# Kernel tuning notes

Hardware: AMD Instinct MI355X
Metric: run time of the kernel (lower is better)

## Reference

```python
import jax, jax.numpy as jnp
import numpy as np

B, C, H, W = 8, 256, 32, 32
N = H * W  # 1024; conv1 maps C -> N channels so all bmms are [B,N,N]


def setup_inputs() -> dict:
    key = jax.random.key(0)
    ks = jax.random.split(key, 11)
    s = 0.02  # weight scale to keep softmax logits in a sane range
    return {
        "x":     jax.random.normal(ks[0], (B, C, H, W), jnp.float32),
        "w1":    jax.random.normal(ks[1], (N, C), jnp.float32) * s,
        "b1":    jax.random.normal(ks[2], (N,), jnp.float32) * s,
        "wq":    jax.random.normal(ks[3], (N, N), jnp.float32) * s,
        "bq":    jax.random.normal(ks[4], (N,), jnp.float32) * s,
        "wv":    jax.random.normal(ks[5], (N, N), jnp.float32) * s,
        "bv":    jax.random.normal(ks[6], (N,), jnp.float32) * s,
        "w2":    jax.random.normal(ks[7], (C, N), jnp.float32) * s,
        "b2":    jax.random.normal(ks[8], (C,), jnp.float32) * s,
        "alpha": jax.random.normal(ks[9], (1,), jnp.float32),
        "beta":  jax.random.normal(ks[10], (1,), jnp.float32),
    }


def reference(x, w1, b1, wq, bq, wv, bv, w2, b2, alpha, beta):
    b, c, h, w = x.shape
    n = h * w
    # 1x1 convs as channel matmuls
    x1 = jnp.einsum('bchw,nc->bnhw', x, w1) + b1[None, :, None, None]  # [B,N,H,W]
    g = (jnp.einsum('bnhw,mn->bmhw', x1, wq) + bq[None, :, None, None]).reshape(b, n, n)
    r = (jnp.einsum('bnhw,mn->bmhw', x1, wv) + bv[None, :, None, None]).reshape(b, n, n)
    xf = x1.reshape(b, n, n)          # m^T in the torch code: [B, N_chan, HW]
    m = xf.transpose(0, 2, 1)         # m: [B, HW, N_chan]
    # spatial attention: z_s = softmax(m^T @ g)
    z_s = jax.nn.softmax(jnp.matmul(xf, g), axis=-1)            # [B,N,N]
    # channel attention: z_c = softmax(g^T @ m)
    z_c = jax.nn.softmax(jnp.matmul(g.transpose(0, 2, 1), m), axis=-1)  # [B,N,N]
    p_s = jnp.matmul(z_s, r)                                    # [B,N,HW]
    p_c = jnp.matmul(z_c, m).transpose(0, 2, 1)                 # [B,N,HW]
    p = (alpha[0] * p_s + beta[0] * p_c).reshape(b, n, h, w)
    out = jnp.einsum('bnhw,cn->bchw', p, w2) + b2[None, :, None, None]
    return out
```

## Files before the change

### kernel.cpp

```cpp
#include <hip/hip_runtime.h>
#include <hip/hip_bf16.h>


typedef __attribute__((ext_vector_type(4))) float f4;
typedef __attribute__((ext_vector_type(8))) short s8;
typedef __attribute__((ext_vector_type(4))) unsigned short us4;
typedef __attribute__((ext_vector_type(8))) unsigned short us8;

__device__ __forceinline__ unsigned short f2bf(float f) {
    __hip_bfloat16 h = __float2bfloat16(f);
    return __builtin_bit_cast(unsigned short, h);
}

#define GAS(p) ((const __attribute__((address_space(1))) unsigned int*)(p))
#define LAS(p) ((__attribute__((address_space(3))) unsigned int*)(p))

__global__ __launch_bounds__(256) void conv_weights(
    const float* __restrict__ w1, const float* __restrict__ wq,
    const float* __restrict__ wv, const float* __restrict__ w2,
    unsigned short* __restrict__ w1b, unsigned short* __restrict__ wqb,
    unsigned short* __restrict__ wvb, unsigned short* __restrict__ w2b,
    const float* __restrict__ bq, const float* __restrict__ bv,
    float* __restrict__ biasqv)
{
    long i = (long)blockIdx.x * 256 + threadIdx.x;
    if (i >= 655360) {
        long j = i - 655360;
        if (j < 512) {
            f4 v = (j < 256) ? ((const f4*)bq)[j] : ((const f4*)bv)[j - 256];
            ((f4*)biasqv)[j] = v;
        }
        return;
    }
    const float* src; unsigned short* dst; long base;
    if (i < 65536)               { src = w1; dst = w1b; base = 0; }
    else if (i < 65536+262144)   { src = wq; dst = wqb; base = 65536; }
    else if (i < 65536+524288)   { src = wv; dst = wvb; base = 65536+262144; }
    else                         { src = w2; dst = w2b; base = 65536+524288; }
    long j = i - base;
    f4 v = ((const f4*)src)[j];
    us4 o;
    #pragma unroll
    for (int k = 0; k < 4; ++k) o[k] = f2bf(v[k]);
    ((us4*)dst)[j] = o;
}

__global__ __launch_bounds__(256) void transpose_x(
    const float* __restrict__ x, unsigned short* __restrict__ xT)
{
    __shared__ float tl[32][33];
    const int b  = blockIdx.z;
    const int q0 = blockIdx.x * 32;
    const int c0 = blockIdx.y * 32;
    const int tx = threadIdx.x & 31, ty = threadIdx.x >> 5;
    #pragma unroll
    for (int j = 0; j < 4; ++j)
        tl[ty + j*8][tx] = x[((long)(b*256 + c0 + ty + j*8))*1024 + q0 + tx];
    __syncthreads();
    #pragma unroll
    for (int j = 0; j < 4; ++j)
        xT[((long)(b*1024 + q0 + ty + j*8))*256 + c0 + tx] = f2bf(tl[tx][ty + j*8]);
}

template<int BIAS, int SPLIT>
__global__ __launch_bounds__(512, 2) void gemm8p(
    const unsigned short* __restrict__ A0, const unsigned short* __restrict__ Bt0,
    int lda, int ldb,
    void* __restrict__ Cv0, void* __restrict__ Cv1, int ldc,
    const float* __restrict__ bias)
{
    constexpr int NT = 16;
    __shared__ __align__(16) unsigned short As[2][2][8192];
    __shared__ __align__(16) unsigned short Bs[2][2][8192];

    const int gx = gridDim.x, gy = gridDim.y;
    const int nwg = gx * gy;
    int d = blockIdx.x + gx * blockIdx.y;
    int swz = (d & 7) * (nwg >> 3) + (d >> 3);
    const int bx = swz % gx;
    const int by = swz / gx;

    const int m0 = by * 256;
    const int n0 = bx * 256;
    const int t  = threadIdx.x;
    const int w  = t >> 6, l = t & 63;
    const int wr = w >> 2, wc = w & 3;
    const int lr = l & 15, lg = l >> 4;

    const unsigned short* Asrc = A0  + (long)m0 * lda;
    const unsigned short* Bsrc = Bt0 + (long)n0 * ldb;

    const int rl4 = l >> 2;
    const int gsw = ((l & 3) ^ ((l >> 3) & 3)) * 8;
    const int rsw = (lr >> 1) & 3;

    auto stage = [&](const unsigned short* src, int ld_, unsigned short* slot,
                     int sp, int kh) {
        #pragma unroll
        for (int i = 0; i < 2; ++i) {
            const int rb = i*128 + w*16;
            __builtin_amdgcn_global_load_lds(
                GAS(src + (long)(rb + rl4)*ld_ + sp*64 + kh*32 + gsw),
                LAS(slot + rb*32), 16, 0, 0);
        }
    };

    f4 acc[8][4];
    #pragma unroll
    for (int i = 0; i < 8; ++i)
        #pragma unroll
        for (int j = 0; j < 4; ++j) acc[i][j] = (f4){0.f, 0.f, 0.f, 0.f};

    s8 aF[4], bF[4];
    auto rdA = [&](int db, int kh, int mh) {
        #pragma unroll
        for (int m = 0; m < 4; ++m) {
            const int R = wr*128 + mh*64 + m*16 + lr;
            aF[m] = *(const s8*)&As[db][kh][R*32 + ((lg ^ rsw) * 8)];
        }
    };
    auto rdB = [&](int db, int kh) {
        #pragma unroll
        for (int n = 0; n < 4; ++n) {
            const int R = wc*64 + n*16 + lr;
            bF[n] = *(const s8*)&Bs[db][kh][R*32 + ((lg ^ rsw) * 8)];
        }
    };

#define MM8(MH)                                                                  \
    __builtin_amdgcn_s_setprio(1);                                               \
    _Pragma("unroll")                                                            \
    for (int m_ = 0; m_ < 4; ++m_)                                               \
        _Pragma("unroll")                                                        \
        for (int n_ = 0; n_ < 4; ++n_)                                           \
            acc[(MH)*4 + m_][n_] = __builtin_amdgcn_mfma_f32_16x16x32_bf16(      \
                aF[m_], bF[n_], acc[(MH)*4 + m_][n_], 0, 0, 0);                  \
    __builtin_amdgcn_s_setprio(0);

#define PH8(DB, KH, MH, RB, STG, VM)                                             \
    rdA(DB, KH, MH);                                                             \
    if (RB) rdB(DB, KH);                                                         \
    STG;                                                                         \
    __builtin_amdgcn_sched_barrier(0);                                           \
    __builtin_amdgcn_s_barrier();                                                \
    asm volatile("s_waitcnt lgkmcnt(0)" ::: "memory");                           \
    __builtin_amdgcn_sched_barrier(0);                                           \
    MM8(MH);                                                                     \
    VM;                                                                          \
    __builtin_amdgcn_s_barrier();

    stage(Asrc, lda, &As[0][0][0], 0, 0);
    stage(Bsrc, ldb, &Bs[0][0][0], 0, 0);
    stage(Asrc, lda, &As[0][1][0], 0, 1);
    stage(Bsrc, ldb, &Bs[0][1][0], 0, 1);
    stage(Asrc, lda, &As[1][0][0], 1, 0);
    stage(Bsrc, ldb, &Bs[1][0][0], 1, 0);
    asm volatile("s_waitcnt vmcnt(4)" ::: "memory");
    __builtin_amdgcn_sched_barrier(0);
    __builtin_amdgcn_s_barrier();

    for (int j = 0; j < NT/2; ++j) {
        const int tb = 2*j + 1;
        const int t2 = (2*j + 2) & (NT - 1);
        const int t3 = (2*j + 3) & (NT - 1);
        PH8(0,0,0, 1, stage(Asrc, lda, &As[1][1][0], tb, 1), (void)0)
        PH8(0,0,1, 0, stage(Bsrc, ldb, &Bs[1][1][0], tb, 1), (void)0)
        PH8(0,1,0, 1, stage(Asrc, lda, &As[0][0][0], t2, 0), (void)0)
        PH8(0,1,1, 0, stage(Bsrc, ldb, &Bs[0][0][0], t2, 0),
            asm volatile("s_waitcnt vmcnt(4)" ::: "memory"))
        PH8(1,0,0, 1, stage(Asrc, lda, &As[0][1][0], t2, 1), (void)0)
        PH8(1,0,1, 0, stage(Bsrc, ldb, &Bs[0][1][0], t2, 1), (void)0)
        PH8(1,1,0, 1, stage(Asrc, lda, &As[1][0][0], t3, 0), (void)0)
        PH8(1,1,1, 0, stage(Bsrc, ldb, &Bs[1][0][0], t3, 0),
            asm volatile("s_waitcnt vmcnt(4)" ::: "memory"))
    }
#undef PH8
#undef MM8

    void* Cd = Cv0; int nbase = n0;
    if (SPLIT && n0 >= 1024) { Cd = Cv1; nbase = n0 - 1024; }

    const int rbase = lg * 4;
    #pragma unroll
    for (int mi = 0; mi < 8; ++mi) {
        #pragma unroll
        for (int n = 0; n < 4; ++n) {
            const int row  = m0 + wr*128 + mi*16 + rbase;
            const int col  = nbase + wc*64 + n*16 + lr;
            const int bcol = n0    + wc*64 + n*16 + lr;
            #pragma unroll
            for (int j = 0; j < 4; ++j) {
                float v = acc[mi][n][j];
                if (BIAS == 2) v += bias[bcol];
                ((unsigned short*)Cd)[(long)(row + j)*ldc + col] = f2bf(v);
            }
        }
    }
}

template<int BIAS, int OUTF32, int SPLIT, int NPASS, int COLSUM>
__global__ __launch_bounds__(512, 2) void gemm256(
    const unsigned short* __restrict__ A0, const unsigned short* __restrict__ Bt0,
    const unsigned short* __restrict__ A1, const unsigned short* __restrict__ Bt1,
    long sA, long sB, int lda, int ldb,
    void* __restrict__ Cv0, void* __restrict__ Cv1, long sC, int ldc,
    const float* __restrict__ bias, int nt1, float* __restrict__ csp)
{
    __shared__ __align__(16) unsigned short As[3][16384];
    __shared__ __align__(16) unsigned short Bs[3][8192];

    const int gx = gridDim.x, gy = gridDim.y;
    const int nwg = gx * gy * gridDim.z;
    int d = blockIdx.x + gx * (blockIdx.y + gy * blockIdx.z);
    int swz = (d & 7) * (nwg >> 3) + (d >> 3);
    const int bx = swz % gx; int tq = swz / gx;
    const int by = tq % gy;  const int bz = tq / gy;

    const int b  = bz;
    const int m0 = by * 256;
    const int n0 = bx * 128;
    const int t  = threadIdx.x;
    const int w  = t >> 6, l = t & 63;
    const int wr = w >> 1, wc = w & 1;
    const int lr = l & 15, lg = l >> 4;

    const unsigned short* A0b = A0  + (long)b * sA;
    const unsigned short* B0b = Bt0 + (long)b * sB;
    const unsigned short* A1b = (NPASS > 1) ? A1  + (long)b * sA : nullptr;
    const unsigned short* B1b = (NPASS > 1) ? Bt1 + (long)b * sB : nullptr;

    const int rl  = l >> 3;
    const int gsw = ((l & 7) ^ (rl & 7)) * 8;

    const int NT = NPASS * nt1;

    auto stageA = [&](int sp, int bf) {
        const unsigned short* Ap = A0b; int kt = sp * 64;
        if (NPASS > 1 && sp >= nt1) { Ap = A1b; kt = (sp - nt1) * 64; }
        #pragma unroll
        for (int i = 0; i < 4; ++i) {
            const int rb = w*32 + i*8;
            __builtin_amdgcn_global_load_lds(GAS(Ap + (long)(m0 + rb + rl)*lda + kt + gsw),
                                             LAS(&As[bf][rb*64]), 16, 0, 0);
        }
    };
    auto stageB = [&](int sp, int bf) {
        const unsigned short* Bp = B0b; int kt = sp * 64;
        if (NPASS > 1 && sp >= nt1) { Bp = B1b; kt = (sp - nt1) * 64; }
        #pragma unroll
        for (int i = 0; i < 2; ++i) {
            const int rb = w*16 + i*8;
            __builtin_amdgcn_global_load_lds(GAS(Bp + (long)(n0 + rb + rl)*ldb + kt + gsw),
                                             LAS(&Bs[bf][rb*64]), 16, 0, 0);
        }
    };

    f4 acc[4][4];
    #pragma unroll
    for (int i = 0; i < 4; ++i)
        #pragma unroll
        for (int j = 0; j < 4; ++j) acc[i][j] = (f4){0.f, 0.f, 0.f, 0.f};

    stageA(0, 0); stageB(0, 0);
    stageA(1, 1); stageB(1, 1);
    asm volatile("s_waitcnt vmcnt(6)" ::: "memory");
    __builtin_amdgcn_sched_barrier(0);
    __builtin_amdgcn_s_barrier();

    s8 a0[4], b0[4], a1f[4], b1f[4];

    #pragma unroll
    for (int m = 0; m < 4; ++m) {
        const int R = wr*64 + m*16 + lr;
        a0[m] = *(const s8*)&As[0][R*64 + ((lg ^ (R & 7)) * 8)];
    }
    #pragma unroll
    for (int n = 0; n < 4; ++n) {
        const int R = wc*64 + n*16 + lr;
        b0[n] = *(const s8*)&Bs[0][R*64 + ((lg ^ (R & 7)) * 8)];
    }
    asm volatile("s_waitcnt lgkmcnt(0)" ::: "memory");
    __builtin_amdgcn_sched_barrier(0);

    int buf = 0;
    for (int s = 0; s < NT; ++s) {
        int bn = buf + 2; if (bn >= 3) bn -= 3;
        int bx1 = buf + 1; if (bx1 >= 3) bx1 -= 3;

        #pragma unroll
        for (int m = 0; m < 4; ++m) {
            const int R = wr*64 + m*16 + lr;
            a1f[m] = *(const s8*)&As[buf][R*64 + (((4 + lg) ^ (R & 7)) * 8)];
        }
        #pragma unroll
        for (int n = 0; n < 4; ++n) {
            const int R = wc*64 + n*16 + lr;
            b1f[n] = *(const s8*)&Bs[buf][R*64 + (((4 + lg) ^ (R & 7)) * 8)];
        }
        if (s + 2 < NT) stageA(s + 2, bn);
        __builtin_amdgcn_s_setprio(1);
        #pragma unroll
        for (int m = 0; m < 4; ++m)
            #pragma unroll
            for (int n = 0; n < 4; ++n)
                acc[m][n] = __builtin_amdgcn_mfma_f32_16x16x32_bf16(a0[m], b0[n], acc[m][n], 0, 0, 0);
        __builtin_amdgcn_s_setprio(0);
        asm volatile("s_waitcnt lgkmcnt(0)" ::: "memory");
        __builtin_amdgcn_sched_barrier(0);

        if (s + 1 < NT) {
            if (s + 2 < NT) asm volatile("s_waitcnt vmcnt(4)" ::: "memory");
            else            asm volatile("s_waitcnt vmcnt(0)" ::: "memory");
            __builtin_amdgcn_sched_barrier(0);
            __builtin_amdgcn_s_barrier();
            #pragma unroll
            for (int m = 0; m < 4; ++m) {
                const int R = wr*64 + m*16 + lr;
                a0[m] = *(const s8*)&As[bx1][R*64 + ((lg ^ (R & 7)) * 8)];
            }
            #pragma unroll
            for (int n = 0; n < 4; ++n) {
                const int R = wc*64 + n*16 + lr;
                b0[n] = *(const s8*)&Bs[bx1][R*64 + ((lg ^ (R & 7)) * 8)];
            }
            if (s + 2 < NT) stageB(s + 2, bn);
            __builtin_amdgcn_s_setprio(1);
            #pragma unroll
            for (int m = 0; m < 4; ++m)
                #pragma unroll
                for (int n = 0; n < 4; ++n)
                    acc[m][n] = __builtin_amdgcn_mfma_f32_16x16x32_bf16(a1f[m], b1f[n], acc[m][n], 0, 0, 0);
            __builtin_amdgcn_s_setprio(0);
            asm volatile("s_waitcnt lgkmcnt(0)" ::: "memory");
            __builtin_amdgcn_sched_barrier(0);
        } else {
            __builtin_amdgcn_s_setprio(1);
            #pragma unroll
            for (int m = 0; m < 4; ++m)
                #pragma unroll
                for (int n = 0; n < 4; ++n)
                    acc[m][n] = __builtin_amdgcn_mfma_f32_16x16x32_bf16(a1f[m], b1f[n], acc[m][n], 0, 0, 0);
            __builtin_amdgcn_s_setprio(0);
        }

        buf = bx1;
    }

    void* Cd = Cv0; int nbase = n0;
    if (SPLIT && n0 >= 1024) { Cd = Cv1; nbase = n0 - 1024; }

    const int rbase = lg * 4;
    #pragma unroll
    for (int m = 0; m < 4; ++m) {
        #pragma unroll
        for (int n = 0; n < 4; ++n) {
            const int row  = m0 + wr*64 + m*16 + rbase;
            const int col  = nbase + wc*64 + n*16 + lr;
            const int bcol = n0    + wc*64 + n*16 + lr;
            #pragma unroll
            for (int j = 0; j < 4; ++j) {
                float v = acc[m][n][j];
                if (BIAS == 1) v += bias[row + j];
                else if (BIAS == 2) v += bias[bcol];
                const long idx = (long)b*sC + (long)(row + j)*ldc + col;
                if (OUTF32) ((float*)Cd)[idx] = v;
                else ((unsigned short*)Cd)[idx] = f2bf(v);
            }
        }
    }

    if (COLSUM) {
        const int p = by*16 + wr*4 + lg;
        #pragma unroll
        for (int n = 0; n < 4; ++n) {
            float s = 0.f;
            #pragma unroll
            for (int m = 0; m < 4; ++m)
                #pragma unroll
                for (int j = 0; j < 4; ++j) s += __expf(acc[m][n][j]);
            const int col = n0 + wc*64 + n*16 + lr;
            csp[(long)p*8192 + b*1024 + col] = s;
        }
    }
}

template<int BIAS, int OUTF32, int NT1, int NBUF>
__global__ __launch_bounds__(256) void gemm_pipe(
    const unsigned short* __restrict__ A0, const unsigned short* __restrict__ Bt0,
    long sA, long sB, int lda, int ldb,
    void* __restrict__ Cv0, long sC, int ldc,
    const float* __restrict__ bias)
{
    constexpr int NT = NT1;
    __shared__ __align__(16) unsigned short As[NBUF][4096];
    __shared__ __align__(16) unsigned short Bs[NBUF][4096];

    const int gx = gridDim.x, gy = gridDim.y;
    const int nwg = gx * gy * gridDim.z;
    int d = blockIdx.x + gx * (blockIdx.y + gy * blockIdx.z);
    int swz = (d & 7) * (nwg >> 3) + (d >> 3);
    const int bx = swz % gx; int tq = swz / gx;
    const int by = tq % gy;  const int bz = tq / gy;

    const int b  = bz;
    const int m0 = by * 128;
    const int n0 = bx * 128;
    const int t  = threadIdx.x;
    const int w  = t >> 6, l = t & 63;
    const int wr = w >> 1, wc = w & 1;
    const int lr = l & 15;

    const unsigned short* A0b = A0  + (long)b * sA;
    const unsigned short* B0b = Bt0 + (long)b * sB;

    const int rA   = w*32 + (l >> 2);
    const int cswz = ((l & 3) ^ ((l >> 3) & 3)) * 8;
    const int swzr = (((l >> 4) ^ ((lr >> 1) & 3)) * 8);

    f4 acc[4][4];
    #pragma unroll
    for (int i = 0; i < 4; ++i)
        #pragma unroll
        for (int j = 0; j < 4; ++j) acc[i][j] = (f4){0.f, 0.f, 0.f, 0.f};

    auto stage = [&](int sp, int bf) {
        const int kt = sp * 32;
        __builtin_amdgcn_global_load_lds(GAS(A0b + (long)(m0 + rA     )*lda + kt + cswz), LAS(&As[bf][w*1024      ]), 16, 0, 0);
        __builtin_amdgcn_global_load_lds(GAS(A0b + (long)(m0 + rA + 16)*lda + kt + cswz), LAS(&As[bf][w*1024 + 512]), 16, 0, 0);
        __builtin_amdgcn_global_load_lds(GAS(B0b + (long)(n0 + rA     )*ldb + kt + cswz), LAS(&Bs[bf][w*1024      ]), 16, 0, 0);
        __builtin_amdgcn_global_load_lds(GAS(B0b + (long)(n0 + rA + 16)*ldb + kt + cswz), LAS(&Bs[bf][w*1024 + 512]), 16, 0, 0);
    };

    #pragma unroll
    for (int dpl = 0; dpl < NBUF - 1; ++dpl) stage(dpl, dpl);

    int buf = 0;
    for (int s = 0; s < NT; ++s) {
        if (NBUF >= 4 && s + 2 < NT) asm volatile("s_waitcnt vmcnt(8)" ::: "memory");
        else if (s + 1 < NT)         asm volatile("s_waitcnt vmcnt(4)" ::: "memory");
        else                         asm volatile("s_waitcnt vmcnt(0)" ::: "memory");
        __builtin_amdgcn_s_barrier();
        __builtin_amdgcn_sched_barrier(0);

        s8 aF[4], bF[4];
        #pragma unroll
        for (int m = 0; m < 4; ++m) aF[m] = *(const s8*)&As[buf][(wr*64 + m*16 + lr)*32 + swzr];
        #pragma unroll
        for (int n = 0; n < 4; ++n) bF[n] = *(const s8*)&Bs[buf][(wc*64 + n*16 + lr)*32 + swzr];

        if (s + NBUF - 1 < NT) {
            int bn = buf + NBUF - 1; if (bn >= NBUF) bn -= NBUF;
            stage(s + NBUF - 1, bn);
        }

        __builtin_amdgcn_s_setprio(1);
        #pragma unroll
        for (int m = 0; m < 4; ++m)
            #pragma unroll
            for (int n = 0; n < 4; ++n)
                acc[m][n] = __builtin_amdgcn_mfma_f32_16x16x32_bf16(aF[m], bF[n], acc[m][n], 0, 0, 0);
        __builtin_amdgcn_s_setprio(0);

        if (++buf == NBUF) buf = 0;
    }

    const int rbase = (l >> 4) * 4;
    #pragma unroll
    for (int m = 0; m < 4; ++m) {
        #pragma unroll
        for (int n = 0; n < 4; ++n) {
            const int row = m0 + wr*64 + m*16 + rbase;
            const int col = n0 + wc*64 + n*16 + lr;
            #pragma unroll
            for (int j = 0; j < 4; ++j) {
                float v = acc[m][n][j];
                if (BIAS == 1) v += bias[row + j];
                else if (BIAS == 2) v += bias[col];
                const long idx = (long)b*sC + (long)(row + j)*ldc + col;
                if (OUTF32) ((float*)Cv0)[idx] = v;
                else ((unsigned short*)Cv0)[idx] = f2bf(v);
            }
        }
    }
}

__global__ __launch_bounds__(256) void row_softmax(
    const float* __restrict__ S, unsigned short* __restrict__ Z,
    const float* __restrict__ scale_p)
{
    const int wid = threadIdx.x >> 6, l = threadIdx.x & 63;
    const long row = (long)blockIdx.x * 4 + wid;
    const float* src = S + row * 1024;
    f4 v[4];
    #pragma unroll
    for (int i = 0; i < 4; ++i) v[i] = *(const f4*)&src[(i*64 + l)*4];
    float m = -3.4e38f;
    #pragma unroll
    for (int i = 0; i < 4; ++i)
        #pragma unroll
        for (int j = 0; j < 4; ++j) m = fmaxf(m, v[i][j]);
    #pragma unroll
    for (int off = 32; off; off >>= 1) m = fmaxf(m, __shfl_xor(m, off));
    float s = 0.f;
    #pragma unroll
    for (int i = 0; i < 4; ++i)
        #pragma unroll
        for (int j = 0; j < 4; ++j) { v[i][j] = __expf(v[i][j] - m); s += v[i][j]; }
    #pragma unroll
    for (int off = 32; off; off >>= 1) s += __shfl_xor(s, off);
    const float c = scale_p[0] / s;
    #pragma unroll
    for (int i = 0; i < 4; ++i) {
        us4 o;
        #pragma unroll
        for (int j = 0; j < 4; ++j) o[j] = f2bf(v[i][j] * c);
        *(us4*)&Z[row*1024 + (long)(i*64 + l)*4] = o;
    }
}

__global__ __launch_bounds__(256) void col_reduce(
    const float* __restrict__ csp, float* __restrict__ cs)
{
    const int q = blockIdx.x * 256 + threadIdx.x;
    float s = 0.f;
    #pragma unroll
    for (int p = 0; p < 64; ++p) s += csp[(long)p*8192 + q];
    cs[q] = s;
}

__global__ __launch_bounds__(256) void col_write(
    const float* __restrict__ S, const float* __restrict__ cs,
    unsigned short* __restrict__ Z, const float* __restrict__ scale_p)
{
    __shared__ float tile[64][65];
    const int b  = blockIdx.z;
    const int q0 = blockIdx.x * 64;
    const int k0 = blockIdx.y * 64;
    const int t  = threadIdx.x;
    const float* Sb = S + (long)b * 1048576;
    const int tq = t & 15, tr = t >> 4;
    #pragma unroll
    for (int ii = 0; ii < 4; ++ii) {
        const int kr = tr + ii*16;
        f4 v = *(const f4*)&Sb[(long)(k0 + kr)*1024 + q0 + tq*4];
        tile[kr][tq*4+0] = v[0]; tile[kr][tq*4+1] = v[1];
        tile[kr][tq*4+2] = v[2]; tile[kr][tq*4+3] = v[3];
    }
    __syncthreads();
    const int qr = t >> 2, kp = t & 3;
    const int q = q0 + qr;
    const float inv = scale_p[0] / cs[b*1024 + q];
    unsigned short* Zb = Z + (long)b*1048576 + (long)q*1024 + k0 + kp*16;
    us8 o0, o1;
    #pragma unroll
    for (int e = 0; e < 8; ++e) o0[e] = f2bf(inv * __expf(tile[kp*16 + e][qr]));
    #pragma unroll
    for (int e = 0; e < 8; ++e) o1[e] = f2bf(inv * __expf(tile[kp*16 + 8 + e][qr]));
    *(us8*)&Zb[0] = o0;
    *(us8*)&Zb[8] = o1;
}

extern "C" void kernel_launch(void* const* d_in, const int* in_sizes, int n_in,
                              void* d_out, int out_size, void* d_ws, size_t ws_size,
                              hipStream_t stream)
{
    const float* x     = (const float*)d_in[0];
    const float* w1    = (const float*)d_in[1];
    const float* b1    = (const float*)d_in[2];
    const float* wq    = (const float*)d_in[3];
    const float* bq    = (const float*)d_in[4];
    const float* wv    = (const float*)d_in[5];
    const float* bv    = (const float*)d_in[6];
    const float* w2    = (const float*)d_in[7];
    const float* b2    = (const float*)d_in[8];
    const float* alpha = (const float*)d_in[9];
    const float* beta  = (const float*)d_in[10];
    float* out = (float*)d_out;

    char* ws = (char*)d_ws;
    size_t off = 0;
    auto alloc = [&](size_t bytes) -> void* {
        void* p = ws + off; off += (bytes + 255) & ~(size_t)255; return p;
    };
    unsigned short* w1b   = (unsigned short*)alloc(1024L*256*2);
    unsigned short* wqvb  = (unsigned short*)alloc(2048L*1024*2);
    unsigned short* w2b   = (unsigned short*)alloc(256L*1024*2);
    float*          biasqv= (float*)alloc(2048L*4);
    float*          cspv  = (float*)alloc(64L*8192*4);
    float*          csv   = (float*)alloc(8L*1024*4);
    unsigned short* xTb   = (unsigned short*)alloc(8L*1024*256*2);
    unsigned short* x1b   = (unsigned short*)alloc(8L*1024*1024*2);
    unsigned short* x1tb  = (unsigned short*)alloc(8L*1024*1024*2);
    unsigned short* gtb   = (unsigned short*)alloc(8L*1024*1024*2);
    unsigned short* rtb   = (unsigned short*)alloc(8L*1024*1024*2);
    float*          Sf    = (float*)alloc(8L*1024*1024*4);
    unsigned short* zsb = x1tb;
    unsigned short* zcb = gtb;
    unsigned short* Ptb = (unsigned short*)Sf;

    const long S1M = 1048576;

    conv_weights<<<2562, 256, 0, stream>>>(w1, wq, wv, w2, w1b, wqvb, wqvb + S1M, w2b, bq, bv, biasqv);
    transpose_x<<<dim3(32, 8, 8), 256, 0, stream>>>(x, xTb);

    gemm256<1,0,0,1,0><<<dim3(8, 4, 8), 512, 0, stream>>>(
        w1b, xTb, nullptr, nullptr, 0, 262144, 256, 256, x1b, nullptr, S1M, 1024, b1, 4, nullptr);
    gemm256<2,0,0,1,0><<<dim3(8, 32, 1), 512, 0, stream>>>(
        xTb, w1b, nullptr, nullptr, 0, 0, 256, 256, x1tb, nullptr, 0, 1024, b1, 4, nullptr);
    gemm8p<2,1><<<dim3(8, 32), 512, 0, stream>>>(
        x1tb, wqvb, 1024, 1024, gtb, rtb, 1024, biasqv);
    gemm256<0,1,0,1,1><<<dim3(8, 4, 8), 512, 0, stream>>>(
        x1b, gtb, nullptr, nullptr, S1M, S1M, 1024, 1024, Sf, nullptr, S1M, 1024, nullptr, 16, cspv);
    row_softmax<<<2048, 256, 0, stream>>>(Sf, zsb, alpha);
    col_reduce<<<32, 256, 0, stream>>>(cspv, csv);
    col_write<<<dim3(16, 16, 8), 256, 0, stream>>>(Sf, csv, zcb, beta);
    gemm256<0,0,0,2,0><<<dim3(8, 4, 8), 512, 0, stream>>>(
        rtb, zsb, zcb, x1b, S1M, S1M, 1024, 1024, Ptb, nullptr, S1M, 1024, nullptr, 16, nullptr);
    gemm_pipe<1,1,32,4><<<dim3(8, 2, 8), 256, 0, stream>>>(
        w2b, Ptb, 0, S1M, 1024, 1024, out, 262144, 1024, b2);
}
```

Before: 175.0 us.

## Fuse exp and softmax stats into score GEMM, defer normalization to dual GEMM

The score GEMM now applies exp in its epilogue, stores bf16 exponentials instead of fp32 scores, and emits partial row and column sums. A small stats_reduce kernel finishes those sums, and a transpose kernel produces the column-softmax operand. A new dual-accumulator GEMM applies the 1/rowsum and 1/colsum scaling, with alpha and beta, in its epilogue. Weight conversion and the x transpose are merged into one launch. This drops the fp32 score round-trip and the separate softmax passes. The risk is that exp without max-subtraction could overflow on larger logits, and the second GEMM now holds two accumulator sets, which raises register pressure.

```diff
diff --git a/kernel.cpp b/kernel.cpp
--- a/kernel.cpp
+++ b/kernel.cpp
@@ -11,55 +11,59 @@
     __hip_bfloat16 h = __float2bfloat16(f);
     return __builtin_bit_cast(unsigned short, h);
 }
+__device__ __forceinline__ float bf2f(unsigned short u) {
+    unsigned int x = ((unsigned int)u) << 16;
+    return __builtin_bit_cast(float, x);
+}
 
 #define GAS(p) ((const __attribute__((address_space(1))) unsigned int*)(p))
 #define LAS(p) ((__attribute__((address_space(3))) unsigned int*)(p))
 
-__global__ __launch_bounds__(256) void conv_weights(
+__global__ __launch_bounds__(256) void prep(
     const float* __restrict__ w1, const float* __restrict__ wq,
     const float* __restrict__ wv, const float* __restrict__ w2,
     unsigned short* __restrict__ w1b, unsigned short* __restrict__ wqb,
     unsigned short* __restrict__ wvb, unsigned short* __restrict__ w2b,
     const float* __restrict__ bq, const float* __restrict__ bv,
-    float* __restrict__ biasqv)
-{
-    long i = (long)blockIdx.x * 256 + threadIdx.x;
-    if (i >= 655360) {
-        long j = i - 655360;
-        if (j < 512) {
-            f4 v = (j < 256) ? ((const f4*)bq)[j] : ((const f4*)bv)[j - 256];
-            ((f4*)biasqv)[j] = v;
-        }
-        return;
-    }
-    const float* src; unsigned short* dst; long base;
-    if (i < 65536)               { src = w1; dst = w1b; base = 0; }
-    else if (i < 65536+262144)   { src = wq; dst = wqb; base = 65536; }
-    else if (i < 65536+524288)   { src = wv; dst = wvb; base = 65536+262144; }
-    else                         { src = w2; dst = w2b; base = 65536+524288; }
-    long j = i - base;
-    f4 v = ((const f4*)src)[j];
-    us4 o;
-    #pragma unroll
-    for (int k = 0; k < 4; ++k) o[k] = f2bf(v[k]);
-    ((us4*)dst)[j] = o;
-}
-
-__global__ __launch_bounds__(256) void transpose_x(
+    float* __restrict__ biasqv,
     const float* __restrict__ x, unsigned short* __restrict__ xT)
 {
     __shared__ float tl[32][33];
-    const int b  = blockIdx.z;
-    const int q0 = blockIdx.x * 32;
-    const int c0 = blockIdx.y * 32;
-    const int tx = threadIdx.x & 31, ty = threadIdx.x >> 5;
-    #pragma unroll
-    for (int j = 0; j < 4; ++j)
-        tl[ty + j*8][tx] = x[((long)(b*256 + c0 + ty + j*8))*1024 + q0 + tx];
-    __syncthreads();
-    #pragma unroll
-    for (int j = 0; j < 4; ++j)
-        xT[((long)(b*1024 + q0 + ty + j*8))*256 + c0 + tx] = f2bf(tl[tx][ty + j*8]);
+    if (blockIdx.x < 2562) {
+        long i = (long)blockIdx.x * 256 + threadIdx.x;
+        if (i >= 655360) {
+            long j = i - 655360;
+            if (j < 512) {
+                f4 v = (j < 256) ? ((const f4*)bq)[j] : ((const f4*)bv)[j - 256];
+                ((f4*)biasqv)[j] = v;
+            }
+            return;
+        }
+        const float* src; unsigned short* dst; long base;
+        if (i < 65536)               { src = w1; dst = w1b; base = 0; }
+        else if (i < 65536+262144)   { src = wq; dst = wqb; base = 65536; }
+        else if (i < 65536+524288)   { src = wv; dst = wvb; base = 65536+262144; }
+        else                         { src = w2; dst = w2b; base = 65536+524288; }
+        long j = i - base;
+        f4 v = ((const f4*)src)[j];
+        us4 o;
+        #pragma unroll
+        for (int k = 0; k < 4; ++k) o[k] = f2bf(v[k]);
+        ((us4*)dst)[j] = o;
+    } else {
+        const int idx = blockIdx.x - 2562;
+        const int q0 = (idx & 31) * 32;
+        const int c0 = ((idx >> 5) & 7) * 32;
+        const int b  = idx >> 8;
+        const int tx = threadIdx.x & 31, ty = threadIdx.x >> 5;
+        #pragma unroll
+        for (int j = 0; j < 4; ++j)
+            tl[ty + j*8][tx] = x[((long)(b*256 + c0 + ty + j*8))*1024 + q0 + tx];
+        __syncthreads();
+        #pragma unroll
+        for (int j = 0; j < 4; ++j)
+            xT[((long)(b*1024 + q0 + ty + j*8))*256 + c0 + tx] = f2bf(tl[tx][ty + j*8]);
+    }
 }
 
 template<int BIAS, int SPLIT>
@@ -198,13 +202,13 @@
     }
 }
 
-template<int BIAS, int OUTF32, int SPLIT, int NPASS, int COLSUM>
+template<int BIAS, int OUTF32, int STATS>
 __global__ __launch_bounds__(512, 2) void gemm256(
     const unsigned short* __restrict__ A0, const unsigned short* __restrict__ Bt0,
-    const unsigned short* __restrict__ A1, const unsigned short* __restrict__ Bt1,
     long sA, long sB, int lda, int ldb,
-    void* __restrict__ Cv0, void* __restrict__ Cv1, long sC, int ldc,
-    const float* __restrict__ bias, int nt1, float* __restrict__ csp)
+    void* __restrict__ Cv0, long sC, int ldc,
+    const float* __restrict__ bias, int nt1,
+    float* __restrict__ csp, float* __restrict__ rsp)
 {
     __shared__ __align__(16) unsigned short As[3][16384];
     __shared__ __align__(16) unsigned short Bs[3][8192];
@@ -226,31 +230,27 @@
 
     const unsigned short* A0b = A0  + (long)b * sA;
     const unsigned short* B0b = Bt0 + (long)b * sB;
-    const unsigned short* A1b = (NPASS > 1) ? A1  + (long)b * sA : nullptr;
-    const unsigned short* B1b = (NPASS > 1) ? Bt1 + (long)b * sB : nullptr;
 
     const int rl  = l >> 3;
     const int gsw = ((l & 7) ^ (rl & 7)) * 8;
 
-    const int NT = NPASS * nt1;
+    const int NT = nt1;
 
     auto stageA = [&](int sp, int bf) {
-        const unsigned short* Ap = A0b; int kt = sp * 64;
-        if (NPASS > 1 && sp >= nt1) { Ap = A1b; kt = (sp - nt1) * 64; }
+        const int kt = sp * 64;
         #pragma unroll
         for (int i = 0; i < 4; ++i) {
             const int rb = w*32 + i*8;
-            __builtin_amdgcn_global_load_lds(GAS(Ap + (long)(m0 + rb + rl)*lda + kt + gsw),
+            __builtin_amdgcn_global_load_lds(GAS(A0b + (long)(m0 + rb + rl)*lda + kt + gsw),
                                              LAS(&As[bf][rb*64]), 16, 0, 0);
         }
     };
     auto stageB = [&](int sp, int bf) {
-        const unsigned short* Bp = B0b; int kt = sp * 64;
-        if (NPASS > 1 && sp >= nt1) { Bp = B1b; kt = (sp - nt1) * 64; }
+        const int kt = sp * 64;
         #pragma unroll
         for (int i = 0; i < 2; ++i) {
             const int rb = w*16 + i*8;
-            __builtin_amdgcn_global_load_lds(GAS(Bp + (long)(n0 + rb + rl)*ldb + kt + gsw),
+            __builtin_amdgcn_global_load_lds(GAS(B0b + (long)(n0 + rb + rl)*ldb + kt + gsw),
                                              LAS(&Bs[bf][rb*64]), 16, 0, 0);
         }
     };
@@ -346,40 +346,228 @@
         buf = bx1;
     }
 
-    void* Cd = Cv0; int nbase = n0;
-    if (SPLIT && n0 >= 1024) { Cd = Cv1; nbase = n0 - 1024; }
-
     const int rbase = lg * 4;
+    float csum[4] = {0.f, 0.f, 0.f, 0.f};
+    float rsum[16];
+    #pragma unroll
+    for (int i = 0; i < 16; ++i) rsum[i] = 0.f;
+
     #pragma unroll
     for (int m = 0; m < 4; ++m) {
         #pragma unroll
         for (int n = 0; n < 4; ++n) {
             const int row  = m0 + wr*64 + m*16 + rbase;
-            const int col  = nbase + wc*64 + n*16 + lr;
-            const int bcol = n0    + wc*64 + n*16 + lr;
+            const int col  = n0 + wc*64 + n*16 + lr;
             #pragma unroll
             for (int j = 0; j < 4; ++j) {
                 float v = acc[m][n][j];
                 if (BIAS == 1) v += bias[row + j];
-                else if (BIAS == 2) v += bias[bcol];
+                else if (BIAS == 2) v += bias[col];
                 const long idx = (long)b*sC + (long)(row + j)*ldc + col;
-                if (OUTF32) ((float*)Cd)[idx] = v;
-                else ((unsigned short*)Cd)[idx] = f2bf(v);
+                if (STATS) {
+                    float ev = __expf(v);
+                    unsigned short bv = f2bf(ev);
+                    ((unsigned short*)Cv0)[idx] = bv;
+                    float evr = bf2f(bv);
+                    csum[n] += evr;
+                    rsum[m*4 + j] += evr;
+                } else if (OUTF32) {
+                    ((float*)Cv0)[idx] = v;
+                } else {
+                    ((unsigned short*)Cv0)[idx] = f2bf(v);
+                }
             }
         }
     }
 
-    if (COLSUM) {
+    if (STATS) {
         const int p = by*16 + wr*4 + lg;
         #pragma unroll
         for (int n = 0; n < 4; ++n) {
-            float s = 0.f;
-            #pragma unroll
-            for (int m = 0; m < 4; ++m)
-                #pragma unroll
-                for (int j = 0; j < 4; ++j) s += __expf(acc[m][n][j]);
             const int col = n0 + wc*64 + n*16 + lr;
-            csp[(long)p*8192 + b*1024 + col] = s;
+            csp[(long)p*8192 + b*1024 + col] = csum[n];
+        }
+        const int p2 = bx*32 + wc*16 + lr;
+        #pragma unroll
+        for (int m = 0; m < 4; ++m)
+            #pragma unroll
+            for (int j = 0; j < 4; ++j) {
+                const int row = m0 + wr*64 + m*16 + rbase + j;
+                rsp[(long)(b*1024 + row)*256 + p2] = rsum[m*4 + j];
+            }
+    }
+}
+
+__global__ __launch_bounds__(512, 2) void gemm_dual2(
+    const unsigned short* __restrict__ A0, const unsigned short* __restrict__ Bt0,
+    const unsigned short* __restrict__ A1, const unsigned short* __restrict__ Bt1,
+    const float* __restrict__ rs, const float* __restrict__ cs,
+    const float* __restrict__ alpha_p, const float* __restrict__ beta_p,
+    unsigned short* __restrict__ C)
+{
+    constexpr int NT = 32;
+    __shared__ __align__(16) unsigned short As[3][16384];
+    __shared__ __align__(16) unsigned short Bs[3][8192];
+
+    const int gx = gridDim.x, gy = gridDim.y;
+    const int nwg = gx * gy * gridDim.z;
+    int d = blockIdx.x + gx * (blockIdx.y + gy * blockIdx.z);
+    int swz = (d & 7) * (nwg >> 3) + (d >> 3);
+    const int bx = swz % gx; int tq = swz / gx;
+    const int by = tq % gy;  const int bz = tq / gy;
+
+    const int b  = bz;
+    const int m0 = by * 256;
+    const int n0 = bx * 128;
+    const int t  = threadIdx.x;
+    const int w  = t >> 6, l = t & 63;
+    const int wr = w >> 1, wc = w & 1;
+    const int lr = l & 15, lg = l >> 4;
+
+    const unsigned short* A0b = A0  + (long)b * 1048576;
+    const unsigned short* B0b = Bt0 + (long)b * 1048576;
+    const unsigned short* A1b = A1  + (long)b * 1048576;
+    const unsigned short* B1b = Bt1 + (long)b * 1048576;
+
+    const int rl  = l >> 3;
+    const int gsw = ((l & 7) ^ (rl & 7)) * 8;
+
+    auto stageA = [&](int sp, int bf) {
+        const unsigned short* Ap = (sp >= 16) ? A1b : A0b;
+        const int kt = ((sp >= 16) ? sp - 16 : sp) * 64;
+        #pragma unroll
+        for (int i = 0; i < 4; ++i) {
+            const int rb = w*32 + i*8;
+            __builtin_amdgcn_global_load_lds(GAS(Ap + (long)(m0 + rb + rl)*1024 + kt + gsw),
+                                             LAS(&As[bf][rb*64]), 16, 0, 0);
+        }
+    };
+    auto stageB = [&](int sp, int bf) {
+        const unsigned short* Bp = (sp >= 16) ? B1b : B0b;
+        const int kt = ((sp >= 16) ? sp - 16 : sp) * 64;
+        #pragma unroll
+        for (int i = 0; i < 2; ++i) {
+            const int rb = w*16 + i*8;
+            __builtin_amdgcn_global_load_lds(GAS(Bp + (long)(n0 + rb + rl)*1024 + kt + gsw),
+                                             LAS(&Bs[bf][rb*64]), 16, 0, 0);
+        }
+    };
+
+    f4 acc1[4][4], acc2[4][4];
+    #pragma unroll
+    for (int i = 0; i < 4; ++i)
+        #pragma unroll
+        for (int j = 0; j < 4; ++j) {
+            acc1[i][j] = (f4){0.f, 0.f, 0.f, 0.f};
+            acc2[i][j] = (f4){0.f, 0.f, 0.f, 0.f};
+        }
+
+    stageA(0, 0); stageB(0, 0);
+    stageA(1, 1); stageB(1, 1);
+    asm volatile("s_waitcnt vmcnt(6)" ::: "memory");
+    __builtin_amdgcn_sched_barrier(0);
+    __builtin_amdgcn_s_barrier();
+
+    s8 a0[4], b0[4], a1f[4], b1f[4];
+
+    #pragma unroll
+    for (int m = 0; m < 4; ++m) {
+        const int R = wr*64 + m*16 + lr;
+        a0[m] = *(const s8*)&As[0][R*64 + ((lg ^ (R & 7)) * 8)];
+    }
+    #pragma unroll
+    for (int n = 0; n < 4; ++n) {
+        const int R = wc*64 + n*16 + lr;
+        b0[n] = *(const s8*)&Bs[0][R*64 + ((lg ^ (R & 7)) * 8)];
+    }
+    asm volatile("s_waitcnt lgkmcnt(0)" ::: "memory");
+    __builtin_amdgcn_sched_barrier(0);
+
+#define DUAL_BODY(ACC)                                                            \
+    {                                                                             \
+        int bn = buf + 2; if (bn >= 3) bn -= 3;                                   \
+        int bx1 = buf + 1; if (bx1 >= 3) bx1 -= 3;                                \
+        _Pragma("unroll")                                                         \
+        for (int m = 0; m < 4; ++m) {                                             \
+            const int R = wr*64 + m*16 + lr;                                      \
+            a1f[m] = *(const s8*)&As[buf][R*64 + (((4 + lg) ^ (R & 7)) * 8)];     \
+        }                                                                         \
+        _Pragma("unroll")                                                         \
+        for (int n = 0; n < 4; ++n) {                                             \
+            const int R = wc*64 + n*16 + lr;                                      \
+            b1f[n] = *(const s8*)&Bs[buf][R*64 + (((4 + lg) ^ (R & 7)) * 8)];     \
+        }                                                                         \
+        if (s + 2 < NT) stageA(s + 2, bn);                                        \
+        __builtin_amdgcn_s_setprio(1);                                            \
+        _Pragma("unroll")                                                         \
+        for (int m = 0; m < 4; ++m)                                               \
+            _Pragma("unroll")                                                     \
+            for (int n = 0; n < 4; ++n)                                           \
+                ACC[m][n] = __builtin_amdgcn_mfma_f32_16x16x32_bf16(a0[m], b0[n], ACC[m][n], 0, 0, 0); \
+        __builtin_amdgcn_s_setprio(0);                                            \
+        asm volatile("s_waitcnt lgkmcnt(0)" ::: "memory");                        \
+        __builtin_amdgcn_sched_barrier(0);                                        \
+        if (s + 1 < NT) {                                                         \
+            if (s + 2 < NT) asm volatile("s_waitcnt vmcnt(4)" ::: "memory");      \
+            else            asm volatile("s_waitcnt vmcnt(0)" ::: "memory");      \
+            __builtin_amdgcn_sched_barrier(0);                                    \
+            __builtin_amdgcn_s_barrier();                                         \
+            _Pragma("unroll")                                                     \
+            for (int m = 0; m < 4; ++m) {                                         \
+                const int R = wr*64 + m*16 + lr;                                  \
+                a0[m] = *(const s8*)&As[bx1][R*64 + ((lg ^ (R & 7)) * 8)];        \
+            }                                                                     \
+            _Pragma("unroll")                                                     \
+            for (int n = 0; n < 4; ++n) {                                         \
+                const int R = wc*64 + n*16 + lr;                                  \
+                b0[n] = *(const s8*)&Bs[bx1][R*64 + ((lg ^ (R & 7)) * 8)];        \
+            }                                                                     \
+            if (s + 2 < NT) stageB(s + 2, bn);                                    \
+            __builtin_amdgcn_s_setprio(1);                                        \
+            _Pragma("unroll")                                                     \
+            for (int m = 0; m < 4; ++m)                                           \
+                _Pragma("unroll")                                                 \
+                for (int n = 0; n < 4; ++n)                                       \
+                    ACC[m][n] = __builtin_amdgcn_mfma_f32_16x16x32_bf16(a1f[m], b1f[n], ACC[m][n], 0, 0, 0); \
+            __builtin_amdgcn_s_setprio(0);                                        \
+            asm volatile("s_waitcnt lgkmcnt(0)" ::: "memory");                    \
+            __builtin_amdgcn_sched_barrier(0);                                    \
+        } else {                                                                  \
+            __builtin_amdgcn_s_setprio(1);                                        \
+            _Pragma("unroll")                                                     \
+            for (int m = 0; m < 4; ++m)                                           \
+                _Pragma("unroll")                                                 \
+                for (int n = 0; n < 4; ++n)                                       \
+                    ACC[m][n] = __builtin_amdgcn_mfma_f32_16x16x32_bf16(a1f[m], b1f[n], ACC[m][n], 0, 0, 0); \
+            __builtin_amdgcn_s_setprio(0);                                        \
+        }                                                                         \
+        buf = bx1;                                                                \
+    }
+
+    int buf = 0;
+    for (int s = 0; s < 16; ++s) DUAL_BODY(acc1)
+    for (int s = 16; s < NT; ++s) DUAL_BODY(acc2)
+#undef DUAL_BODY
+
+    const float al = alpha_p[0], be = beta_p[0];
+    const int rbase = lg * 4;
+    float rscv[4];
+    #pragma unroll
+    for (int n = 0; n < 4; ++n)
+        rscv[n] = al / rs[b*1024 + n0 + wc*64 + n*16 + lr];
+
+    #pragma unroll
+    for (int m = 0; m < 4; ++m) {
+        #pragma unroll
+        for (int j = 0; j < 4; ++j) {
+            const int row = m0 + wr*64 + m*16 + rbase + j;
+            const float csc = be / cs[b*1024 + row];
+            #pragma unroll
+            for (int n = 0; n < 4; ++n) {
+                const int col = n0 + wc*64 + n*16 + lr;
+                float v = acc1[m][n][j]*rscv[n] + acc2[m][n][j]*csc;
+                C[(long)b*1048576 + (long)row*1024 + col] = f2bf(v);
+            }
         }
     }
 }
@@ -484,80 +672,58 @@
     }
 }
 
-__global__ __launch_bounds__(256) void row_softmax(
-    const float* __restrict__ S, unsigned short* __restrict__ Z,
-    const float* __restrict__ scale_p)
+__global__ __launch_bounds__(256) void stats_reduce(
+    const float* __restrict__ csp, const float* __restrict__ rsp,
+    float* __restrict__ cs, float* __restrict__ rs)
 {
-    const int wid = threadIdx.x >> 6, l = threadIdx.x & 63;
-    const long row = (long)blockIdx.x * 4 + wid;
-    const float* src = S + row * 1024;
-    f4 v[4];
-    #pragma unroll
-    for (int i = 0; i < 4; ++i) v[i] = *(const f4*)&src[(i*64 + l)*4];
-    float m = -3.4e38f;
-    #pragma unroll
-    for (int i = 0; i < 4; ++i)
-        #pragma unroll
-        for (int j = 0; j < 4; ++j) m = fmaxf(m, v[i][j]);
-    #pragma unroll
-    for (int off = 32; off; off >>= 1) m = fmaxf(m, __shfl_xor(m, off));
-    float s = 0.f;
-    #pragma unroll
-    for (int i = 0; i < 4; ++i)
-        #pragma unroll
-        for (int j = 0; j < 4; ++j) { v[i][j] = __expf(v[i][j] - m); s += v[i][j]; }
-    #pragma unroll
-    for (int off = 32; off; off >>= 1) s += __shfl_xor(s, off);
-    const float c = scale_p[0] / s;
-    #pragma unroll
-    for (int i = 0; i < 4; ++i) {
-        us4 o;
-        #pragma unroll
-        for (int j = 0; j < 4; ++j) o[j] = f2bf(v[i][j] * c);
-        *(us4*)&Z[row*1024 + (long)(i*64 + l)*4] = o;
-    }
-}
-
-__global__ __launch_bounds__(256) void col_reduce(
-    const float* __restrict__ csp, float* __restrict__ cs)
+    if (blockIdx.x < 32) {
+        const int q = blockIdx.x * 256 + threadIdx.x;
+        float s = 0.f;
+        #pragma unroll
+        for (int p = 0; p < 64; ++p) s += csp[(long)p*8192 + q];
+        cs[q] = s;
+    } else {
+        const int blk = blockIdx.x - 32;
+        const int w = threadIdx.x >> 6, l = threadIdx.x & 63;
+        #pragma unroll
+        for (int i = 0; i < 4; ++i) {
+            const int row = blk*16 + w*4 + i;
+            f4 v = *(const f4*)&rsp[(long)row*256 + l*4];
+            float s = v[0] + v[1] + v[2] + v[3];
+            #pragma unroll
+            for (int off = 32; off; off >>= 1) s += __shfl_xor(s, off);
+            if (l == 0) rs[row] = s;
+        }
+    }
+}
+
+__global__ __launch_bounds__(256) void et_trans(
+    const unsigned short* __restrict__ E, unsigned short* __restrict__ Et)
 {
-    const int q = blockIdx.x * 256 + threadIdx.x;
-    float s = 0.f;
-    #pragma unroll
-    for (int p = 0; p < 64; ++p) s += csp[(long)p*8192 + q];
-    cs[q] = s;
-}
-
-__global__ __launch_bounds__(256) void col_write(
-    const float* __restrict__ S, const float* __restrict__ cs,
-    unsigned short* __restrict__ Z, const float* __restrict__ scale_p)
-{
-    __shared__ float tile[64][65];
+    __shared__ unsigned short tile[64][65];
     const int b  = blockIdx.z;
-    const int q0 = blockIdx.x * 64;
-    const int k0 = blockIdx.y * 64;
+    const int i0 = blockIdx.x * 64;
+    const int q0 = blockIdx.y * 64;
     const int t  = threadIdx.x;
-    const float* Sb = S + (long)b * 1048576;
-    const int tq = t & 15, tr = t >> 4;
-    #pragma unroll
-    for (int ii = 0; ii < 4; ++ii) {
-        const int kr = tr + ii*16;
-        f4 v = *(const f4*)&Sb[(long)(k0 + kr)*1024 + q0 + tq*4];
-        tile[kr][tq*4+0] = v[0]; tile[kr][tq*4+1] = v[1];
-        tile[kr][tq*4+2] = v[2]; tile[kr][tq*4+3] = v[3];
+    const int ch = t & 7, r = t >> 3;
+    const unsigned short* Eb = E + (long)b * 1048576;
+    #pragma unroll
+    for (int pp = 0; pp < 2; ++pp) {
+        const int rr = r + pp*32;
+        us8 v = *(const us8*)&Eb[(long)(i0 + rr)*1024 + q0 + ch*8];
+        #pragma unroll
+        for (int e = 0; e < 8; ++e) tile[rr][ch*8 + e] = v[e];
     }
     __syncthreads();
-    const int qr = t >> 2, kp = t & 3;
-    const int q = q0 + qr;
-    const float inv = scale_p[0] / cs[b*1024 + q];
-    unsigned short* Zb = Z + (long)b*1048576 + (long)q*1024 + k0 + kp*16;
-    us8 o0, o1;
-    #pragma unroll
-    for (int e = 0; e < 8; ++e) o0[e] = f2bf(inv * __expf(tile[kp*16 + e][qr]));
-    #pragma unroll
-    for (int e = 0; e < 8; ++e) o1[e] = f2bf(inv * __expf(tile[kp*16 + 8 + e][qr]));
-    *(us8*)&Zb[0] = o0;
-    *(us8*)&Zb[8] = o1;
+    unsigned short* Etb = Et + (long)b * 1048576;
+    #pragma unroll
+    for (int pp = 0; pp < 2; ++pp) {
+        const int qr = r + pp*32;
+        us8 o;
+        #pragma unroll
+        for (int e = 0; e < 8; ++e) o[e] = tile[ch*8 + e][qr];
+        *(us8*)&Etb[(long)(q0 + qr)*1024 + i0 + ch*8] = o;
+    }
 }
 
 extern "C" void kernel_launch(void* const* d_in, const int* in_sizes, int n_in,
@@ -587,35 +753,35 @@
     unsigned short* w2b   = (unsigned short*)alloc(256L*1024*2);
     float*          biasqv= (float*)alloc(2048L*4);
     float*          cspv  = (float*)alloc(64L*8192*4);
+    float*          rspv  = (float*)alloc(8192L*256*4);
     float*          csv   = (float*)alloc(8L*1024*4);
+    float*          rsv   = (float*)alloc(8L*1024*4);
     unsigned short* xTb   = (unsigned short*)alloc(8L*1024*256*2);
     unsigned short* x1b   = (unsigned short*)alloc(8L*1024*1024*2);
     unsigned short* x1tb  = (unsigned short*)alloc(8L*1024*1024*2);
     unsigned short* gtb   = (unsigned short*)alloc(8L*1024*1024*2);
     unsigned short* rtb   = (unsigned short*)alloc(8L*1024*1024*2);
-    float*          Sf    = (float*)alloc(8L*1024*1024*4);
-    unsigned short* zsb = x1tb;
-    unsigned short* zcb = gtb;
-    unsigned short* Ptb = (unsigned short*)Sf;
+    unsigned short* Ptb   = (unsigned short*)alloc(8L*1024*1024*2);
+    unsigned short* Eb  = x1tb;
+    unsigned short* Etb = gtb;
 
     const long S1M = 1048576;
 
-    conv_weights<<<2562, 256, 0, stream>>>(w1, wq, wv, w2, w1b, wqvb, wqvb + S1M, w2b, bq, bv, biasqv);
-    transpose_x<<<dim3(32, 8, 8), 256, 0, stream>>>(x, xTb);
-
-    gemm256<1,0,0,1,0><<<dim3(8, 4, 8), 512, 0, stream>>>(
-        w1b, xTb, nullptr, nullptr, 0, 262144, 256, 256, x1b, nullptr, S1M, 1024, b1, 4, nullptr);
-    gemm256<2,0,0,1,0><<<dim3(8, 32, 1), 512, 0, stream>>>(
-        xTb, w1b, nullptr, nullptr, 0, 0, 256, 256, x1tb, nullptr, 0, 1024, b1, 4, nullptr);
+    prep<<<4610, 256, 0, stream>>>(w1, wq, wv, w2, w1b, wqvb, wqvb + S1M, w2b,
+                                   bq, bv, biasqv, x, xTb);
+
+    gemm256<1,0,0><<<dim3(8, 4, 8), 512, 0, stream>>>(
+        w1b, xTb, 0, 262144, 256, 256, x1b, S1M, 1024, b1, 4, nullptr, nullptr);
+    gemm256<2,0,0><<<dim3(8, 32, 1), 512, 0, stream>>>(
+        xTb, w1b, 0, 0, 256, 256, x1tb, 0, 1024, b1, 4, nullptr, nullptr);
     gemm8p<2,1><<<dim3(8, 32), 512, 0, stream>>>(
         x1tb, wqvb, 1024, 1024, gtb, rtb, 1024, biasqv);
-    gemm256<0,1,0,1,1><<<dim3(8, 4, 8), 512, 0, stream>>>(
-        x1b, gtb, nullptr, nullptr, S1M, S1M, 1024, 1024, Sf, nullptr, S1M, 1024, nullptr, 16, cspv);
-    row_softmax<<<2048, 256, 0, stream>>>(Sf, zsb, alpha);
-    col_reduce<<<32, 256, 0, stream>>>(cspv, csv);
-    col_write<<<dim3(16, 16, 8), 256, 0, stream>>>(Sf, csv, zcb, beta);
-    gemm256<0,0,0,2,0><<<dim3(8, 4, 8), 512, 0, stream>>>(
-        rtb, zsb, zcb, x1b, S1M, S1M, 1024, 1024, Ptb, nullptr, S1M, 1024, nullptr, 16, nullptr);
+    gemm256<0,0,1><<<dim3(8, 4, 8), 512, 0, stream>>>(
+        x1b, gtb, S1M, S1M, 1024, 1024, Eb, S1M, 1024, nullptr, 16, cspv, rspv);
+    stats_reduce<<<544, 256, 0, stream>>>(cspv, rspv, csv, rsv);
+    et_trans<<<dim3(16, 16, 8), 256, 0, stream>>>(Eb, Etb);
+    gemm_dual2<<<dim3(8, 4, 8), 512, 0, stream>>>(
+        rtb, Eb, Etb, x1b, rsv, csv, alpha, beta, Ptb);
     gemm_pipe<1,1,32,4><<<dim3(8, 2, 8), 256, 0, stream>>>(
         w2b, Ptb, 0, S1M, 1024, 1024, out, 262144, 1024, b2);
 }
```

After: 160.6 us, median of 2. 1.09x faster.
